# Performance work log

Hardware: AMD Instinct MI355X
Metric: run time of the kernel (lower is better)

Reference implementation:

```python
import jax, jax.numpy as jnp
import numpy as np

B, T, D, H, N, S, FF = 8, 1024, 512, 8, 256, 256, 2048
AUD, TXT = 768, 256  # audio_input_dim, text_feature_dim (hardcoded in module)
EPS = 1e-5


def _ln(x, g, b):
    m = x.mean(-1, keepdims=True)
    v = ((x - m) ** 2).mean(-1, keepdims=True)
    return (x - m) / jnp.sqrt(v + EPS) * g + b


def _lin(x, w, b):
    return x @ w + b


def setup_inputs() -> dict:
    keys = iter(jax.random.split(jax.random.key(0), 64))
    def rn(shape, s=0.02):
        return jax.random.normal(next(keys), shape, jnp.float32) * s
    inp = {
        'x': jax.random.normal(next(keys), (B, T, D), jnp.float32),
        'xf': jax.random.normal(next(keys), (B, AUD), jnp.float32),
        'xw': jax.random.normal(next(keys), (B, N, TXT), jnp.float32),
        'xs': jax.random.normal(next(keys), (B, S, D), jnp.float32),
        # feat_proj (linear variant)
        'fp_w': rn((D, D)), 'fp_b': rn((D,)),
        # self-attention
        'sa_ng': 1.0 + rn((D,)), 'sa_nb': rn((D,)),
        'sa_qw': rn((D, D)), 'sa_qb': rn((D,)),
        'sa_kw': rn((D, D)), 'sa_kb': rn((D,)),
        'sa_vw': rn((D, D)), 'sa_vb': rn((D,)),
        'sa_ow': rn((D, D)), 'sa_ob': rn((D,)),
        # cross-attention
        'ca_ng': 1.0 + rn((D,)), 'ca_nb': rn((D,)),
        'ca_tng': 1.0 + rn((D,)), 'ca_tnb': rn((D,)),
        'ca_sng': 1.0 + rn((D,)), 'ca_snb': rn((D,)),
        'ca_qw': rn((D, D)), 'ca_qb': rn((D,)),
        'ca_kw': rn((D, D)), 'ca_kb': rn((D,)),
        'ca_vw': rn((D, D)), 'ca_vb': rn((D,)),
        'ca_apw': rn((AUD, TXT)), 'ca_apb': rn((TXT,)),
        'ca_atw': rn((TXT, D)), 'ca_atb': rn((D,)),
        'ca_ow': rn((D, D)), 'ca_ob': rn((D,)),
        'an_g': 1.0 + rn((D,)), 'an_b': rn((D,)),
        # FFN
        'ffn_w1': rn((D, FF)), 'ffn_b1': rn((FF,)),
        'ffn_w2': rn((FF, D)), 'ffn_b2': rn((D,)),
        'ffn_ng': 1.0 + rn((D,)), 'ffn_nb': rn((D,)),
        'ffn_ow': rn((D, D)), 'ffn_ob': rn((D,)),
    }
    return inp


def reference(x, xf, xw, xs, fp_w, fp_b, sa_ng, sa_nb, sa_qw, sa_qb, sa_kw, sa_kb,
              sa_vw, sa_vb, sa_ow, sa_ob, ca_ng, ca_nb, ca_tng, ca_tnb, ca_sng, ca_snb,
              ca_qw, ca_qb, ca_kw, ca_kb, ca_vw, ca_vb, ca_apw, ca_apb, ca_atw, ca_atb,
              ca_ow, ca_ob, an_g, an_b, ffn_w1, ffn_b1, ffn_w2, ffn_b2, ffn_ng, ffn_nb,
              ffn_ow, ffn_ob):
    Bx, Tx, Dx = x.shape
    dh = Dx // H
    # feat_proj + detached residual (x_ori = x.detach().clone())
    xp = _lin(x, fp_w, fp_b) + jax.lax.stop_gradient(x)

    # ---- self-attention block ----
    xn = _ln(xp, sa_ng, sa_nb)
    q = _lin(xn, sa_qw, sa_qb).reshape(Bx, Tx, H, dh)
    k = _lin(xn, sa_kw, sa_kb).reshape(Bx, Tx, H, dh)
    v = _lin(xn, sa_vw, sa_vb).reshape(Bx, Tx, H, dh)
    scores = jnp.einsum('bthd,bshd->bths', q, k) / jnp.sqrt(jnp.float32(dh))
    ao = jnp.einsum('bths,bshd->bthd', jax.nn.softmax(scores, -1), v).reshape(Bx, Tx, Dx)
    sa_out = xp + _lin(jax.nn.silu(ao), sa_ow, sa_ob)
    y1 = _ln(sa_out + xp, an_g, an_b)

    # ---- cross-attention block (linear attention over text/audio + semantic) ----
    Nw = xw.shape[1]
    xf_p = _lin(xf, ca_apw, ca_apb)                              # [B, 256]
    xf_e = jnp.broadcast_to(xf_p[:, None, :], (Bx, Nw, TXT))
    xw_xf = _lin(jnp.concatenate([xw, xf_e], axis=1), ca_atw, ca_atb)  # [B, 2N, D]
    tn = _ln(xw_xf, ca_tng, ca_tnb)
    sn = _ln(xs, ca_sng, ca_snb)
    cq = jax.nn.softmax(_lin(_ln(y1, ca_ng, ca_nb), ca_qw, ca_qb).reshape(Bx, Tx, H, dh), -1)
    ck = jax.nn.softmax(_lin(tn, ca_kw, ca_kb).reshape(Bx, 2 * Nw, H, dh), 1)
    sk = jax.nn.softmax(_lin(sn, ca_kw, ca_kb).reshape(Bx, -1, H, dh), 1)
    cv = _lin(tn, ca_vw, ca_vb).reshape(Bx, 2 * Nw, H, dh)
    sv = _lin(sn, ca_vw, ca_vb).reshape(Bx, -1, H, dh)
    att = jnp.einsum('bnhd,bnhl->bhdl', ck, cv)                  # [B,H,dh,dh]
    satt = jnp.einsum('bshd,bshl->bhsl', sk, sv)                 # [B,H,S,dh]
    cy = jnp.einsum('bthd,bhdl->bthl', cq, att).reshape(Bx, Tx, Dx)
    sy = jnp.einsum('bthd,bhsl->bthl', cq, satt).reshape(Bx, Tx, Dx)
    ca_out = y1 + _lin(jax.nn.silu(cy + sy), ca_ow, ca_ob)
    y2 = _ln(ca_out + y1, an_g, an_b)

    # ---- FFN block ----
    h = jax.nn.gelu(_lin(y2, ffn_w1, ffn_b1), approximate=False)
    h = _ln(_lin(h, ffn_w2, ffn_b2), ffn_ng, ffn_nb)
    ffn_out = y2 + _lin(jax.nn.silu(h), ffn_ow, ffn_ob)
    y3 = _ln(ffn_out + y2, an_g, an_b)
    return y3
```

## Files before the change

### kernel.cpp

```cpp
#include <hip/hip_runtime.h>
#include <math.h>

typedef unsigned short u16;
typedef short s16x8 __attribute__((ext_vector_type(8)));
typedef float f32x4 __attribute__((ext_vector_type(4)));
typedef unsigned short u16x8 __attribute__((ext_vector_type(8)));
typedef unsigned short u16x4 __attribute__((ext_vector_type(4)));

#define DD 512

__device__ __forceinline__ float silu_f(float x) { return x / (1.f + __expf(-x)); }
__device__ __forceinline__ float gelu_f(float x) {
  float y = 1.5957691216f * (x + 0.044715f * x * x * x);
  return x / (1.f + __expf(-y));
}
__device__ __forceinline__ u16 f2bf(float f) {
  unsigned u = __float_as_uint(f);
  return (u16)((u + 0x7fffu + ((u >> 16) & 1u)) >> 16);
}
__device__ __forceinline__ float bf2f(u16 u) { return __uint_as_float(((unsigned)u) << 16); }
__device__ __forceinline__ unsigned cvtpk_bf16(float a, float b) {
  unsigned r;
  asm("v_cvt_pk_bf16_f32 %0, %1, %2" : "=v"(r) : "v"(a), "v"(b));
  return r;
}

__device__ __forceinline__ void gload16(const void* g, void* l) {
  __builtin_amdgcn_global_load_lds(
      (const __attribute__((address_space(1))) void*)(g),
      (__attribute__((address_space(3))) void*)(l), 16, 0, 0);
}

template<int ACT, int OB>
__global__ __launch_bounds__(256) void gemm64(
    const u16* __restrict__ A, const u16* __restrict__ Bt,
    const float* __restrict__ bias, const float* __restrict__ res, float res_scale,
    float* __restrict__ outf, float* __restrict__ outf2,
    u16* __restrict__ outb, u16* __restrict__ outb2,
    int M, int N, int K)
{
  __shared__ u16 As[2][4096];
  __shared__ u16 Bs[2][4096];
  const int t = threadIdx.x, l = t & 63, w = t >> 6;
  const int gx = gridDim.x;
  const int nblk = gx * gridDim.y;
  const int id = blockIdx.y * gx + blockIdx.x;
  const int nid = (id & 7) * (nblk >> 3) + (id >> 3);
  const int bm = (nid / gx) << 6, bn = (nid % gx) << 6;
  const int wr = (w >> 1) << 5, wc = (w & 1) << 5;
  f32x4 acc[2][2];
#pragma unroll
  for (int i = 0; i < 2; ++i)
#pragma unroll
    for (int j = 0; j < 2; ++j) acc[i][j] = (f32x4){0.f, 0.f, 0.f, 0.f};

  auto stage = [&](int k0, int buf) {
#pragma unroll
    for (int i = 0; i < 2; ++i) {
      int c = t + (i << 8);
      int row = c >> 3, cq = c & 7;
      int cs = cq ^ (row & 7);
      gload16(A + (size_t)(bm + row) * K + k0 + cs * 8, (char*)As[buf] + (i << 12) + (w << 10));
      gload16(Bt + (size_t)(bn + row) * K + k0 + cs * 8, (char*)Bs[buf] + (i << 12) + (w << 10));
    }
  };
  stage(0, 0);
  asm volatile("s_waitcnt vmcnt(0)" ::: "memory");
  __builtin_amdgcn_s_barrier();

  const int fr = l & 15, q0 = l >> 4;
  const int nk = K >> 6;
  int cur = 0;
  for (int kt = 0; kt < nk; ++kt) {
    if (kt + 1 < nk) stage((kt + 1) << 6, cur ^ 1);
    s16x8 af[2][2], bg[2][2];
#pragma unroll
    for (int kk = 0; kk < 2; ++kk)
#pragma unroll
      for (int i = 0; i < 2; ++i) {
        int ra = wr + i * 16 + fr;
        af[kk][i] = *(const s16x8*)&As[cur][ra * 64 + (((q0 + kk * 4)) ^ (ra & 7)) * 8];
        int rb = wc + i * 16 + fr;
        bg[kk][i] = *(const s16x8*)&Bs[cur][rb * 64 + (((q0 + kk * 4)) ^ (rb & 7)) * 8];
      }
    asm volatile("s_waitcnt lgkmcnt(0)" ::: "memory");
    __builtin_amdgcn_sched_barrier(0);
#pragma unroll
    for (int kk = 0; kk < 2; ++kk)
#pragma unroll
      for (int mi = 0; mi < 2; ++mi)
#pragma unroll
        for (int ni = 0; ni < 2; ++ni)
          acc[mi][ni] = __builtin_amdgcn_mfma_f32_16x16x32_bf16(af[kk][mi], bg[kk][ni], acc[mi][ni], 0, 0, 0);
    asm volatile("s_waitcnt vmcnt(0)" ::: "memory");
    __builtin_amdgcn_s_barrier();
    cur ^= 1;
  }

  const int cr0 = (l >> 4) << 2, cc = l & 15;

  if (OB == 0 || OB == 4) {
    float* fdst = outf;
    int coff = bn, ld = N;
    if (OB == 4) { ld = 512; coff = bn & 511; if (bn >= 512) fdst = outf2; }
#pragma unroll
    for (int ni = 0; ni < 2; ++ni) {
      int n = bn + wc + ni * 16 + cc;
      int col = coff + wc + ni * 16 + cc;
      float bia = bias[n];
#pragma unroll
      for (int mi = 0; mi < 2; ++mi) {
#pragma unroll
        for (int r = 0; r < 4; ++r) {
          int m = bm + wr + mi * 16 + cr0 + r;
          size_t off = (size_t)m * ld + col;
          float o = acc[mi][ni][r] + bia;
          if (ACT == 1) o = gelu_f(o);
          if (res) o = fmaf(res_scale, res[off], o);
          fdst[off] = o;
        }
      }
    }
  } else {
    int seg = bn >> 9;
    int colbase = bn & 511;
    if (seg < 2) {
      u16* dst = seg ? outb2 : outb;
#pragma unroll
      for (int ni = 0; ni < 2; ++ni) {
        int col = colbase + wc + ni * 16 + cc;
        float bia = bias[bn + wc + ni * 16 + cc];
#pragma unroll
        for (int mi = 0; mi < 2; ++mi) {
#pragma unroll
          for (int r = 0; r < 4; ++r) {
            int m = bm + wr + mi * 16 + cr0 + r;
            dst[(size_t)m * 512 + col] = f2bf(acc[mi][ni][r] + bia);
          }
        }
      }
    } else {
      u16* tile = &As[0][0];
      __syncthreads();
#pragma unroll
      for (int ni = 0; ni < 2; ++ni) {
        int lc = wc + ni * 16 + cc;
        float bia = bias[bn + wc + ni * 16 + cc];
#pragma unroll
        for (int mi = 0; mi < 2; ++mi) {
          int lm0 = wr + mi * 16 + cr0;
          u16x4 pk;
#pragma unroll
          for (int r = 0; r < 4; ++r) pk[r] = f2bf(acc[mi][ni][r] + bia);
          *(u16x4*)&tile[lc * 64 + (lm0 ^ ((lc & 7) << 3))] = pk;
        }
      }
      __syncthreads();
      int h = colbase >> 6;
      size_t vrow0 = ((size_t)((bm >> 10) * 8 + h)) * 64;
      int d = t >> 3, c8 = (t & 7) << 3;
      *(u16x8*)(((u16*)outf) + (vrow0 + d) * 1024 + (bm & 1023) + c8) =
          *(u16x8*)&tile[d * 64 + (c8 ^ ((d & 7) << 3))];
    }
  }
}

template<int ACT, int OBF>
__global__ __launch_bounds__(512) void gemm8w(
    const u16* __restrict__ A, const u16* __restrict__ Bt,
    const float* __restrict__ bias, float* __restrict__ outf, u16* __restrict__ outb,
    int M, int N, int K)
{
  __shared__ u16 As[2][4096];
  __shared__ u16 Bs[2][8192];
  const int t = threadIdx.x, l = t & 63, w = t >> 6;
  const int gx = gridDim.x;
  const int nblk = gx * gridDim.y;
  const int id = blockIdx.y * gx + blockIdx.x;
  const int nid = (id & 7) * (nblk >> 3) + (id >> 3);
  const int bm = (nid / gx) << 7, bn = (nid % gx) << 8;
  const int wr = (w >> 2) << 6, wc = (w & 3) << 6;
  f32x4 acc[4][4];
#pragma unroll
  for (int i = 0; i < 4; ++i)
#pragma unroll
    for (int j = 0; j < 4; ++j) acc[i][j] = (f32x4){0.f, 0.f, 0.f, 0.f};

  auto stage = [&](int k0, int buf) {
    {
      int row = t >> 2, kq = (t & 3) << 3;
      gload16(A + (size_t)(bm + row) * K + k0 + kq, (char*)As[buf] + (w << 10));
    }
#pragma unroll
    for (int i = 0; i < 2; ++i) {
      int c = t + (i << 9);
      int row = c >> 2, kq = (c & 3) << 3;
      gload16(Bt + (size_t)(bn + row) * K + k0 + kq, (char*)Bs[buf] + ((w + (i << 3)) << 10));
    }
  };
  stage(0, 0);
  asm volatile("s_waitcnt vmcnt(0)" ::: "memory");
  __builtin_amdgcn_s_barrier();

  const int fr = l & 15, fk = (l >> 4) << 3;
  const int nk = K >> 5;
  int cur = 0;
  for (int kt = 0; kt < nk; ++kt) {
    if (kt + 1 < nk) stage((kt + 1) << 5, cur ^ 1);
    s16x8 af[4], bg[4];
#pragma unroll
    for (int i = 0; i < 4; ++i) {
      af[i] = *(const s16x8*)&As[cur][(wr + i * 16 + fr) * 32 + fk];
      bg[i] = *(const s16x8*)&Bs[cur][(wc + i * 16 + fr) * 32 + fk];
    }
    asm volatile("s_waitcnt lgkmcnt(0)" ::: "memory");
    __builtin_amdgcn_sched_barrier(0);
#pragma unroll
    for (int mi = 0; mi < 4; ++mi)
#pragma unroll
      for (int ni = 0; ni < 4; ++ni)
        acc[mi][ni] = __builtin_amdgcn_mfma_f32_16x16x32_bf16(af[mi], bg[ni], acc[mi][ni], 0, 0, 0);
    asm volatile("s_waitcnt vmcnt(0)" ::: "memory");
    __builtin_amdgcn_s_barrier();
    cur ^= 1;
  }

  const int cr0 = (l >> 4) << 2, cc = l & 15;
#pragma unroll
  for (int ni = 0; ni < 4; ++ni) {
    int n = bn + wc + ni * 16 + cc;
    float bia = bias[n];
#pragma unroll
    for (int mi = 0; mi < 4; ++mi) {
#pragma unroll
      for (int r = 0; r < 4; ++r) {
        int m = bm + wr + mi * 16 + cr0 + r;
        size_t off = (size_t)m * N + n;
        float o = acc[mi][ni][r] + bia;
        if (ACT == 1) o = gelu_f(o);
        if (OBF) outb[off] = f2bf(o);
        else outf[off] = o;
      }
    }
  }
}

__global__ __launch_bounds__(256) void xfp_k(
    const float* __restrict__ xf, const u16* __restrict__ apwT,
    const float* __restrict__ bias, float* __restrict__ xfp)
{
  int wid = blockIdx.x * 4 + (threadIdx.x >> 6);
  int lane = threadIdx.x & 63;
  int b = wid >> 8, n = wid & 255;
  const u16* wp = apwT + (size_t)n * 768;
  const float* xp = xf + (size_t)b * 768;
  float s = 0.f;
#pragma unroll
  for (int j = 0; j < 12; ++j) s = fmaf(xp[lane + j * 64], bf2f(wp[lane + j * 64]), s);
#pragma unroll
  for (int m = 1; m < 64; m <<= 1) s += __shfl_xor(s, m);
  if (lane == 0) xfp[wid] = s + bias[n];
}

__global__ __launch_bounds__(256) void biascat_k(
    const float* __restrict__ qb, const float* __restrict__ kb, const float* __restrict__ vb,
    const float* __restrict__ ckb, const float* __restrict__ cvb,
    float* __restrict__ bQKV, float* __restrict__ bKV)
{
  int t = blockIdx.x * 256 + threadIdx.x;
  if (t < 512) bQKV[t] = qb[t];
  else if (t < 1024) bQKV[t] = kb[t - 512];
  else if (t < 1536) bQKV[t] = vb[t - 1024];
  else if (t < 2048) bKV[t - 1536] = ckb[t - 1536];
  else if (t < 2560) bKV[t - 1536] = cvb[t - 2048];
}

__global__ __launch_bounds__(256) void ln_k(
    const float* __restrict__ src, const float* __restrict__ g,
    const float* __restrict__ b, float* __restrict__ out32, u16* __restrict__ out16,
    int rows, int do_silu)
{
  int lane = threadIdx.x & 63, wv = threadIdx.x >> 6;
  int row = (blockIdx.x << 2) + wv;
  if (row >= rows) return;
  const float* p = src + (size_t)row * DD;
  float4 v0 = *(const float4*)(p + lane * 4);
  float4 v1 = *(const float4*)(p + 256 + lane * 4);
  float s = v0.x + v0.y + v0.z + v0.w + v1.x + v1.y + v1.z + v1.w;
  float ss = v0.x*v0.x + v0.y*v0.y + v0.z*v0.z + v0.w*v0.w
           + v1.x*v1.x + v1.y*v1.y + v1.z*v1.z + v1.w*v1.w;
#pragma unroll
  for (int m = 1; m < 64; m <<= 1) { s += __shfl_xor(s, m); ss += __shfl_xor(ss, m); }
  float mean = s * (1.f / 512.f);
  float var = ss * (1.f / 512.f) - mean * mean;
  float rstd = rsqrtf(var + 1e-5f);
  float4 g0 = *(const float4*)(g + lane * 4);
  float4 g1 = *(const float4*)(g + 256 + lane * 4);
  float4 b0 = *(const float4*)(b + lane * 4);
  float4 b1 = *(const float4*)(b + 256 + lane * 4);
  float o[8];
  o[0] = (v0.x - mean) * rstd * g0.x + b0.x;
  o[1] = (v0.y - mean) * rstd * g0.y + b0.y;
  o[2] = (v0.z - mean) * rstd * g0.z + b0.z;
  o[3] = (v0.w - mean) * rstd * g0.w + b0.w;
  o[4] = (v1.x - mean) * rstd * g1.x + b1.x;
  o[5] = (v1.y - mean) * rstd * g1.y + b1.y;
  o[6] = (v1.z - mean) * rstd * g1.z + b1.z;
  o[7] = (v1.w - mean) * rstd * g1.w + b1.w;
  if (do_silu) {
#pragma unroll
    for (int j = 0; j < 8; ++j) o[j] = silu_f(o[j]);
  }
  if (out32) {
    *(float4*)(out32 + (size_t)row * DD + lane * 4) = make_float4(o[0], o[1], o[2], o[3]);
    *(float4*)(out32 + (size_t)row * DD + 256 + lane * 4) = make_float4(o[4], o[5], o[6], o[7]);
  }
  if (out16) {
    u16x4 h0, h1;
#pragma unroll
    for (int j = 0; j < 4; ++j) { h0[j] = f2bf(o[j]); h1[j] = f2bf(o[4 + j]); }
    *(u16x4*)(out16 + (size_t)row * DD + lane * 4) = h0;
    *(u16x4*)(out16 + (size_t)row * DD + 256 + lane * 4) = h1;
  }
}

__global__ __launch_bounds__(256) void attn3_k(
    const u16* __restrict__ q, const u16* __restrict__ k,
    const u16* __restrict__ vt, u16* __restrict__ out)
{
  __shared__ __align__(16) char KVb[2][2][8192];
  __shared__ __align__(16) char QP[16384];
  __shared__ float Lr[4][32];

  const int t = threadIdx.x, l = t & 63, w = t >> 6;
  const int id = blockIdx.x;
  const int blk = (id & 7) * 64 + (id >> 3);
  const int qt = blk & 7, h = (blk >> 3) & 7, b = blk >> 6;
  const size_t qbase = ((size_t)(b * 1024 + qt * 128)) * 512 + h * 64;
  const size_t kbase = ((size_t)(b * 1024)) * 512 + h * 64;
  const size_t vbase = ((size_t)((b * 8 + h) * 64)) * 1024;

#pragma unroll
  for (int i = 0; i < 4; ++i) {
    int chunk = i * 256 + w * 64 + l;
    int row = chunk >> 3, c = chunk & 7;
    int cs = c ^ (row & 7);
    gload16(q + qbase + (size_t)row * 512 + cs * 8, QP + (i * 256 + w * 64) * 16);
  }
  auto stageKV = [&](int st, int buf) {
#pragma unroll
    for (int i = 0; i < 2; ++i) {
      int chunk = i * 256 + w * 64 + l;
      int row = chunk >> 3, c = chunk & 7;
      int cs = c ^ (row & 7);
      gload16(k + kbase + (size_t)(st * 64 + row) * 512 + cs * 8,
              KVb[buf][0] + (i * 256 + w * 64) * 16);
      gload16(vt + vbase + (size_t)row * 1024 + st * 64 + cs * 8,
              KVb[buf][1] + (i * 256 + w * 64) * 16);
    }
  };
  stageKV(0, 0);
  __syncthreads();

  s16x8 qf[2][2];
#pragma unroll
  for (int ti = 0; ti < 2; ++ti)
#pragma unroll
    for (int kk = 0; kk < 2; ++kk) {
      int row = w * 32 + ti * 16 + (l & 15);
      int ch = ((l >> 4) + kk * 4) ^ (row & 7);
      qf[ti][kk] = *(const s16x8*)(QP + row * 128 + ch * 16);
    }

  f32x4 oacc[2][4];
#pragma unroll
  for (int qi = 0; qi < 2; ++qi)
#pragma unroll
    for (int dj = 0; dj < 4; ++dj) oacc[qi][dj] = (f32x4){0.f, 0.f, 0.f, 0.f};
  float lsum[2] = {0.f, 0.f};

  int cur = 0;
  for (int st = 0; st < 16; ++st) {
    if (st + 1 < 16) stageKV(st + 1, cur ^ 1);
    f32x4 sacc[4][2];
#pragma unroll
    for (int si = 0; si < 4; ++si)
#pragma unroll
      for (int ti = 0; ti < 2; ++ti) sacc[si][ti] = (f32x4){0.f, 0.f, 0.f, 0.f};
#pragma unroll
    for (int si = 0; si < 4; ++si) {
#pragma unroll
      for (int kk = 0; kk < 2; ++kk) {
        int s = si * 16 + (l & 15);
        int ch = ((l >> 4) + kk * 4) ^ (s & 7);
        s16x8 kf = *(const s16x8*)(KVb[cur][0] + s * 128 + ch * 16);
#pragma unroll
        for (int ti = 0; ti < 2; ++ti)
          sacc[si][ti] = __builtin_amdgcn_mfma_f32_16x16x32_bf16(kf, qf[ti][kk], sacc[si][ti], 0, 0, 0);
      }
    }
#pragma unroll
    for (int si = 0; si < 4; ++si)
#pragma unroll
      for (int ti = 0; ti < 2; ++ti) {
        float e0 = __expf(sacc[si][ti][0] * 0.125f);
        float e1 = __expf(sacc[si][ti][1] * 0.125f);
        float e2 = __expf(sacc[si][ti][2] * 0.125f);
        float e3 = __expf(sacc[si][ti][3] * 0.125f);
        lsum[ti] += (e0 + e1) + (e2 + e3);
        uint2 pk2;
        pk2.x = cvtpk_bf16(e0, e1);
        pk2.y = cvtpk_bf16(e2, e3);
        int tl = ti * 16 + (l & 15);
        int sb = (si * 16 + (l >> 4) * 4) * 2;
        *(uint2*)(QP + w * 4096 + tl * 128 + (sb ^ ((tl & 7) << 4))) = pk2;
      }
#pragma unroll
    for (int kk = 0; kk < 2; ++kk) {
      s16x8 pf[2];
#pragma unroll
      for (int qi = 0; qi < 2; ++qi) {
        int tl = qi * 16 + (l & 15);
        int ch = ((l >> 4) + kk * 4) ^ (tl & 7);
        pf[qi] = *(const s16x8*)(QP + w * 4096 + tl * 128 + ch * 16);
      }
#pragma unroll
      for (int dj = 0; dj < 4; ++dj) {
        int d = dj * 16 + (l & 15);
        int ch = ((l >> 4) + kk * 4) ^ (d & 7);
        s16x8 vf = *(const s16x8*)(KVb[cur][1] + d * 128 + ch * 16);
#pragma unroll
        for (int qi = 0; qi < 2; ++qi)
          oacc[qi][dj] = __builtin_amdgcn_mfma_f32_16x16x32_bf16(pf[qi], vf, oacc[qi][dj], 0, 0, 0);
      }
    }
    cur ^= 1;
    __syncthreads();
  }

#pragma unroll
  for (int ti = 0; ti < 2; ++ti) {
    lsum[ti] += __shfl_xor(lsum[ti], 16);
    lsum[ti] += __shfl_xor(lsum[ti], 32);
    Lr[w][ti * 16 + (l & 15)] = lsum[ti];
  }
  __syncthreads();
  u16* otile = (u16*)QP;
#pragma unroll
  for (int qi = 0; qi < 2; ++qi) {
    float linv[4];
#pragma unroll
    for (int r = 0; r < 4; ++r) linv[r] = 1.f / Lr[w][qi * 16 + (l >> 4) * 4 + r];
#pragma unroll
    for (int dj = 0; dj < 4; ++dj) {
#pragma unroll
      for (int r = 0; r < 4; ++r) {
        int trl = w * 32 + qi * 16 + (l >> 4) * 4 + r;
        otile[trl * 64 + dj * 16 + (l & 15)] = f2bf(silu_f(oacc[qi][dj][r] * linv[r]));
      }
    }
  }
  __syncthreads();
#pragma unroll
  for (int p = 0; p < 4; ++p) {
    int flat = p * 256 + t;
    int row = flat >> 3, c8 = (flat & 7) << 3;
    *(u16x8*)(out + ((size_t)(b * 1024 + qt * 128 + row)) * 512 + h * 64 + c8) =
        *(u16x8*)&otile[row * 64 + c8];
  }
}

__global__ __launch_bounds__(256) void softmax64_k(float* __restrict__ p, int rows)
{
  int lane = threadIdx.x & 63, wv = threadIdx.x >> 6;
  int row = (blockIdx.x << 2) + wv;
  if (row >= rows) return;
  float x = p[(size_t)row * 64 + lane];
  float m = x;
#pragma unroll
  for (int mk = 1; mk < 64; mk <<= 1) m = fmaxf(m, __shfl_xor(m, mk));
  float e = __expf(x - m);
  float s = e;
#pragma unroll
  for (int mk = 1; mk < 64; mk <<= 1) s += __shfl_xor(s, mk);
  p[(size_t)row * 64 + lane] = e / s;
}

template<int NL>
__global__ __launch_bounds__(256) void smseq_k(float* __restrict__ p)
{
  __shared__ float red[256];
  int t = threadIdx.x;
  int ci = t & 15, nj = t >> 4;
  int b = blockIdx.x >> 5, cg = blockIdx.x & 31;
  int col = cg * 16 + ci;
  float vals[NL / 16];
  float s = 0.f;
#pragma unroll
  for (int j = 0; j < NL / 16; ++j) {
    float x = __expf(p[((size_t)(b * NL) + nj + j * 16) * 512 + col]);
    vals[j] = x; s += x;
  }
  red[t] = s;
  __syncthreads();
  float tot = 0.f;
#pragma unroll
  for (int j = 0; j < 16; ++j) tot += red[ci + j * 16];
  float inv = 1.f / tot;
#pragma unroll
  for (int j = 0; j < NL / 16; ++j)
    p[((size_t)(b * NL) + nj + j * 16) * 512 + col] = vals[j] * inv;
}

__global__ __launch_bounds__(256) void build_xc_k(
    const float* __restrict__ xw, const float* __restrict__ xfp, u16* __restrict__ xc)
{
  int idx = blockIdx.x * 256 + threadIdx.x;
  int c = idx & 255, n = (idx >> 8) & 511, b = idx >> 17;
  float val = (n < 256) ? xw[((b << 8) + n) * 256 + c] : xfp[(b << 8) + c];
  xc[idx] = f2bf(val);
}

__global__ __launch_bounds__(256) void attmat1_k(
    const float* __restrict__ ckp, const float* __restrict__ cvp, float* __restrict__ attp)
{
  __shared__ float a_s[64][68];
  __shared__ float b_s[64][68];
  int bh = blockIdx.x >> 3, sl = blockIdx.x & 7;
  int h = bh & 7, b = bh >> 3;
  int n0 = sl << 6;
  int tid = threadIdx.x;
  int d = tid & 63, lg = tid >> 6;
  float acc[16];
#pragma unroll
  for (int j = 0; j < 16; ++j) acc[j] = 0.f;
#pragma unroll
  for (int i = 0; i < 4; ++i) {
    int f = tid + (i << 8);
    int row = f >> 4, c4 = (f & 15) << 2;
    size_t src = ((size_t)(b * 512 + n0 + row)) * DD + h * 64 + c4;
    *(float4*)&a_s[row][c4] = *(const float4*)(ckp + src);
    *(float4*)&b_s[row][c4] = *(const float4*)(cvp + src);
  }
  __syncthreads();
  for (int nn = 0; nn < 64; ++nn) {
    float av = a_s[nn][d];
#pragma unroll
    for (int j4 = 0; j4 < 4; ++j4) {
      float4 b4 = *(float4*)&b_s[nn][lg * 16 + j4 * 4];
      acc[j4*4+0] = fmaf(av, b4.x, acc[j4*4+0]);
      acc[j4*4+1] = fmaf(av, b4.y, acc[j4*4+1]);
      acc[j4*4+2] = fmaf(av, b4.z, acc[j4*4+2]);
      acc[j4*4+3] = fmaf(av, b4.w, acc[j4*4+3]);
    }
  }
  float* op = attp + ((size_t)(bh * 8 + sl)) * 4096 + d * 64 + lg * 16;
#pragma unroll
  for (int j4 = 0; j4 < 4; ++j4)
    *(float4*)(op + j4 * 4) = make_float4(acc[j4*4+0], acc[j4*4+1], acc[j4*4+2], acc[j4*4+3]);
}

__global__ __launch_bounds__(256) void attred_k(
    const float* __restrict__ attp, float* __restrict__ att)
{
  int idx = (blockIdx.x * 256 + threadIdx.x) * 4;
  int bh = idx >> 12, e = idx & 4095;
  float4 s = make_float4(0.f, 0.f, 0.f, 0.f);
#pragma unroll
  for (int sl = 0; sl < 8; ++sl) {
    float4 v = *(const float4*)&attp[((size_t)(bh * 8 + sl)) * 4096 + e];
    s.x += v.x; s.y += v.y; s.z += v.z; s.w += v.w;
  }
  *(float4*)&att[idx] = s;
}

__global__ __launch_bounds__(256) void rowsum64_k(
    const float* __restrict__ skp, float* __restrict__ r)
{
  int wv = threadIdx.x >> 6, l = threadIdx.x & 63;
  int g16 = l >> 4, l16 = l & 15;
  for (int it = 0; it < 16; ++it) {
    int rid = blockIdx.x * 256 + wv * 64 + it * 4 + g16;
    const float* base = skp + (size_t)(rid >> 3) * 512 + (rid & 7) * 64;
    float4 v = *(const float4*)(base + l16 * 4);
    float s = (v.x + v.y) + (v.z + v.w);
    s += __shfl_xor(s, 1); s += __shfl_xor(s, 2);
    s += __shfl_xor(s, 4); s += __shfl_xor(s, 8);
    if (l16 == 0) r[rid] = s;
  }
}

__global__ __launch_bounds__(256) void sy2_k(
    const float* __restrict__ r, const float* __restrict__ svp, float* __restrict__ sy)
{
  __shared__ float part[4][64];
  int b = blockIdx.x >> 3, h = blockIdx.x & 7;
  int t = threadIdx.x;
  int li = t & 63, sg = t >> 6;
  float acc = 0.f;
  for (int j = 0; j < 64; ++j) {
    int s = sg * 64 + j;
    size_t ix = (size_t)(b * 256 + s);
    acc = fmaf(r[ix * 8 + h], svp[ix * 512 + h * 64 + li], acc);
  }
  part[sg][li] = acc;
  __syncthreads();
  if (t < 64) sy[(b * 8 + h) * 64 + t] = (part[0][t] + part[1][t]) + (part[2][t] + part[3][t]);
}

__global__ __launch_bounds__(256) void cy_k(
    const float* __restrict__ cq, const float* __restrict__ att,
    const float* __restrict__ sy, u16* __restrict__ out)
{
  __shared__ float atts[64][68];
  __shared__ float qs[64][68];
  __shared__ float sys[64];
  int blk = blockIdx.x;
  int tt = blk & 15, h = (blk >> 4) & 7, b = blk >> 7;
  int t0 = tt << 6;
  int tid = threadIdx.x;
#pragma unroll
  for (int i = 0; i < 4; ++i) {
    int f = tid + (i << 8);
    int row = f >> 4, c4 = (f & 15) << 2;
    *(float4*)&atts[row][c4] = *(const float4*)(att + (size_t)(b * 8 + h) * 4096 + row * 64 + c4);
    *(float4*)&qs[row][c4] = *(const float4*)(cq + ((size_t)(b * 1024 + t0 + row)) * DD + h * 64 + c4);
  }
  if (tid < 64) sys[tid] = sy[(b * 8 + h) * 64 + tid];
  __syncthreads();
  int r = tid >> 2, lg = tid & 3;
  float acc[16];
#pragma unroll
  for (int j = 0; j < 16; ++j) acc[j] = 0.f;
  for (int d = 0; d < 64; ++d) {
    float qv = qs[r][d];
#pragma unroll
    for (int j4 = 0; j4 < 4; ++j4) {
      float4 a4 = *(float4*)&atts[d][lg * 16 + j4 * 4];
      acc[j4*4+0] = fmaf(qv, a4.x, acc[j4*4+0]);
      acc[j4*4+1] = fmaf(qv, a4.y, acc[j4*4+1]);
      acc[j4*4+2] = fmaf(qv, a4.z, acc[j4*4+2]);
      acc[j4*4+3] = fmaf(qv, a4.w, acc[j4*4+3]);
    }
  }
  u16* op = out + ((size_t)(b * 1024 + t0 + r)) * DD + h * 64 + lg * 16;
#pragma unroll
  for (int j4 = 0; j4 < 4; ++j4) {
    u16x4 o4;
    o4[0] = f2bf(silu_f(acc[j4*4+0] + sys[lg * 16 + j4*4+0]));
    o4[1] = f2bf(silu_f(acc[j4*4+1] + sys[lg * 16 + j4*4+1]));
    o4[2] = f2bf(silu_f(acc[j4*4+2] + sys[lg * 16 + j4*4+2]));
    o4[3] = f2bf(silu_f(acc[j4*4+3] + sys[lg * 16 + j4*4+3]));
    *(u16x4*)(op + j4 * 4) = o4;
  }
}

__global__ __launch_bounds__(256) void cvtf2b_k(const float* __restrict__ in, u16* __restrict__ out, int n)
{
  int i = (blockIdx.x * 256 + threadIdx.x) * 4;
  if (i >= n) return;
  float4 v = *(const float4*)(in + i);
  u16x4 o;
  o[0] = f2bf(v.x); o[1] = f2bf(v.y); o[2] = f2bf(v.z); o[3] = f2bf(v.w);
  *(u16x4*)(out + i) = o;
}

__global__ __launch_bounds__(256) void wtrans_k(const float* __restrict__ W, u16* __restrict__ Wt, int Kd, int Nd)
{
  __shared__ float tile[32][33];
  int ntn = Nd >> 5;
  int tk = blockIdx.x / ntn, tn = blockIdx.x % ntn;
  int lx = threadIdx.x & 31, ly = threadIdx.x >> 5;
#pragma unroll
  for (int i = 0; i < 4; ++i)
    tile[ly + 8 * i][lx] = W[(size_t)(tk * 32 + ly + 8 * i) * Nd + tn * 32 + lx];
  __syncthreads();
#pragma unroll
  for (int i = 0; i < 4; ++i)
    Wt[(size_t)(tn * 32 + ly + 8 * i) * Kd + tk * 32 + lx] = f2bf(tile[lx][ly + 8 * i]);
}

struct W10 { const float* w[10]; u16* o[10]; };
__global__ __launch_bounds__(256) void wtrans10_k(W10 p)
{
  __shared__ float tile[32][33];
  int wi = blockIdx.x >> 8;
  int tb = blockIdx.x & 255;
  int tk = tb >> 4, tn = tb & 15;
  const float* W = p.w[wi];
  u16* Wt = p.o[wi];
  int lx = threadIdx.x & 31, ly = threadIdx.x >> 5;
#pragma unroll
  for (int i = 0; i < 4; ++i)
    tile[ly + 8 * i][lx] = W[(size_t)(tk * 32 + ly + 8 * i) * 512 + tn * 32 + lx];
  __syncthreads();
#pragma unroll
  for (int i = 0; i < 4; ++i)
    Wt[(size_t)(tn * 32 + ly + 8 * i) * 512 + tk * 32 + lx] = f2bf(tile[lx][ly + 8 * i]);
}

extern "C" void kernel_launch(void* const* d_in, const int* in_sizes, int n_in,
                              void* d_out, int out_size, void* d_ws, size_t ws_size,
                              hipStream_t stream)
{
  const float* x      = (const float*)d_in[0];
  const float* xf     = (const float*)d_in[1];
  const float* xw     = (const float*)d_in[2];
  const float* xs     = (const float*)d_in[3];
  const float* fp_w   = (const float*)d_in[4];
  const float* fp_b   = (const float*)d_in[5];
  const float* sa_ng  = (const float*)d_in[6];
  const float* sa_nb  = (const float*)d_in[7];
  const float* sa_qw  = (const float*)d_in[8];
  const float* sa_qb  = (const float*)d_in[9];
  const float* sa_kw  = (const float*)d_in[10];
  const float* sa_kb  = (const float*)d_in[11];
  const float* sa_vw  = (const float*)d_in[12];
  const float* sa_vb  = (const float*)d_in[13];
  const float* sa_ow  = (const float*)d_in[14];
  const float* sa_ob  = (const float*)d_in[15];
  const float* ca_ng  = (const float*)d_in[16];
  const float* ca_nb  = (const float*)d_in[17];
  const float* ca_tng = (const float*)d_in[18];
  const float* ca_tnb = (const float*)d_in[19];
  const float* ca_sng = (const float*)d_in[20];
  const float* ca_snb = (const float*)d_in[21];
  const float* ca_qw  = (const float*)d_in[22];
  const float* ca_qb  = (const float*)d_in[23];
  const float* ca_kw  = (const float*)d_in[24];
  const float* ca_kb  = (const float*)d_in[25];
  const float* ca_vw  = (const float*)d_in[26];
  const float* ca_vb  = (const float*)d_in[27];
  const float* ca_apw = (const float*)d_in[28];
  const float* ca_apb = (const float*)d_in[29];
  const float* ca_atw = (const float*)d_in[30];
  const float* ca_atb = (const float*)d_in[31];
  const float* ca_ow  = (const float*)d_in[32];
  const float* ca_ob  = (const float*)d_in[33];
  const float* an_g   = (const float*)d_in[34];
  const float* an_b   = (const float*)d_in[35];
  const float* ffn_w1 = (const float*)d_in[36];
  const float* ffn_b1 = (const float*)d_in[37];
  const float* ffn_w2 = (const float*)d_in[38];
  const float* ffn_b2 = (const float*)d_in[39];
  const float* ffn_ng = (const float*)d_in[40];
  const float* ffn_nb = (const float*)d_in[41];
  const float* ffn_ow = (const float*)d_in[42];
  const float* ffn_ob = (const float*)d_in[43];

  float* ws = (float*)d_ws;
  float* slotZ = ws;
  float* slotP = ws + 4194304;
  u16* S1 = (u16*)(ws + 8388608);
  u16* S2 = (u16*)(ws + 10485760);
  u16* S3 = (u16*)(ws + 12582912);
  u16* S4 = (u16*)(ws + 14680064);
  u16* Vt = (u16*)(ws + 16777216);
  u16* S6 = (u16*)(ws + 18874368);
  float* ck  = ws + 20971520;
  float* sk  = ws + 23068672;
  float* cv  = ws + 24117248;
  float* sv  = ws + 26214400;
  float* tnr = ws + 27262976;
  u16* tn = (u16*)(ws + 29360128);
  u16* sn = (u16*)(ws + 30408704);
  u16* h1 = (u16*)(ws + 20971520);
  u16* xc = (u16*)(ws + 30932992);
  float* att = ws + 31457280;
  float* xfp = ws + 31719424;
  float* sy  = ws + 31723520;
  u16* wb = (u16*)(ws + 31727616);
  u16* fp_wt   = wb;
  u16* sa_qwt  = wb + 262144;
  u16* sa_kwt  = wb + 524288;
  u16* sa_vwt  = wb + 786432;
  u16* sa_owt  = wb + 1048576;
  u16* ca_qwt  = wb + 1310720;
  u16* ca_kwt  = wb + 1572864;
  u16* ca_vwt  = wb + 1835008;
  u16* ca_owt  = wb + 2097152;
  u16* ffn_owt = wb + 2359296;
  u16* ca_atwt = wb + 2621440;
  u16* ffn_w1t = wb + 2752512;
  u16* ffn_w2t = wb + 3801088;
  u16* apwT    = wb + 4849664;
  float* bQKV  = (float*)(wb + 5046272);
  float* bKV   = bQKV + 1536;
  float* attp  = ws + 34260992;
  float* rws   = ws + 36358144;

  dim3 blk(256);
  auto g64 = [](int M, int N) { return dim3((unsigned)(N >> 6), (unsigned)(M >> 6)); };

  cvtf2b_k<<<dim3(4096), blk, 0, stream>>>(x, S1, 4194304);
  W10 wp;
  wp.w[0] = fp_w;  wp.o[0] = fp_wt;
  wp.w[1] = sa_qw; wp.o[1] = sa_qwt;
  wp.w[2] = sa_kw; wp.o[2] = sa_kwt;
  wp.w[3] = sa_vw; wp.o[3] = sa_vwt;
  wp.w[4] = sa_ow; wp.o[4] = sa_owt;
  wp.w[5] = ca_qw; wp.o[5] = ca_qwt;
  wp.w[6] = ca_kw; wp.o[6] = ca_kwt;
  wp.w[7] = ca_vw; wp.o[7] = ca_vwt;
  wp.w[8] = ca_ow; wp.o[8] = ca_owt;
  wp.w[9] = ffn_ow; wp.o[9] = ffn_owt;
  wtrans10_k<<<dim3(2560), blk, 0, stream>>>(wp);
  wtrans_k<<<dim3(128), blk, 0, stream>>>(ca_atw, ca_atwt, 256, 512);
  wtrans_k<<<dim3(1024), blk, 0, stream>>>(ffn_w1, ffn_w1t, 512, 2048);
  wtrans_k<<<dim3(1024), blk, 0, stream>>>(ffn_w2, ffn_w2t, 2048, 512);
  wtrans_k<<<dim3(192), blk, 0, stream>>>(ca_apw, apwT, 768, 256);
  biascat_k<<<dim3(10), blk, 0, stream>>>(sa_qb, sa_kb, sa_vb, ca_kb, ca_vb, bQKV, bKV);

  xfp_k<<<dim3(512), blk, 0, stream>>>(xf, apwT, ca_apb, xfp);
  build_xc_k<<<dim3(4096), blk, 0, stream>>>(xw, xfp, xc);
  gemm64<0,0><<<g64(4096, 512), blk, 0, stream>>>(xc, ca_atwt, ca_atb, nullptr, 0.f, tnr, nullptr, nullptr, nullptr, 4096, 512, 256);
  ln_k<<<dim3(1024), blk, 0, stream>>>(tnr, ca_tng, ca_tnb, nullptr, tn, 4096, 0);
  ln_k<<<dim3(512), blk, 0, stream>>>(xs, ca_sng, ca_snb, nullptr, sn, 2048, 0);

  gemm64<0,0><<<g64(8192, 512), blk, 0, stream>>>(S1, fp_wt, fp_b, x, 1.f, slotP, nullptr, nullptr, nullptr, 8192, 512, 512);
  ln_k<<<dim3(2048), blk, 0, stream>>>(slotP, sa_ng, sa_nb, nullptr, S2, 8192, 0);
  gemm64<0,3><<<g64(8192, 1536), blk, 0, stream>>>(S2, sa_qwt, bQKV, nullptr, 0.f, (float*)Vt, nullptr, S3, S4, 8192, 1536, 512);
  attn3_k<<<dim3(512), blk, 0, stream>>>(S3, S4, Vt, S6);
  gemm64<0,0><<<g64(8192, 512), blk, 0, stream>>>(S6, sa_owt, sa_ob, slotP, 2.f, slotZ, nullptr, nullptr, nullptr, 8192, 512, 512);
  ln_k<<<dim3(2048), blk, 0, stream>>>(slotZ, an_g, an_b, slotP, nullptr, 8192, 0);

  ln_k<<<dim3(2048), blk, 0, stream>>>(slotP, ca_ng, ca_nb, nullptr, S1, 8192, 0);
  gemm64<0,0><<<g64(8192, 512), blk, 0, stream>>>(S1, ca_qwt, ca_qb, nullptr, 0.f, slotZ, nullptr, nullptr, nullptr, 8192, 512, 512);
  softmax64_k<<<dim3(16384), blk, 0, stream>>>(slotZ, 65536);
  gemm64<0,4><<<g64(6144, 1024), blk, 0, stream>>>(tn, ca_kwt, bKV, nullptr, 0.f, ck, cv, nullptr, nullptr, 6144, 1024, 512);
  smseq_k<512><<<dim3(256), blk, 0, stream>>>(ck);
  smseq_k<256><<<dim3(256), blk, 0, stream>>>(sk);
  attmat1_k<<<dim3(512), blk, 0, stream>>>(ck, cv, attp);
  attred_k<<<dim3(256), blk, 0, stream>>>(attp, att);
  rowsum64_k<<<dim3(64), blk, 0, stream>>>(sk, rws);
  sy2_k<<<dim3(64), blk, 0, stream>>>(rws, sv, sy);
  cy_k<<<dim3(1024), blk, 0, stream>>>(slotZ, att, sy, S2);
  gemm64<0,0><<<g64(8192, 512), blk, 0, stream>>>(S2, ca_owt, ca_ob, slotP, 2.f, slotZ, nullptr, nullptr, nullptr, 8192, 512, 512);
  ln_k<<<dim3(2048), blk, 0, stream>>>(slotZ, an_g, an_b, slotP, S3, 8192, 0);

  gemm8w<1,1><<<dim3(8, 64), dim3(512), 0, stream>>>(S3, ffn_w1t, ffn_b1, nullptr, h1, 8192, 2048, 512);
  gemm64<0,0><<<g64(8192, 512), blk, 0, stream>>>(h1, ffn_w2t, ffn_b2, nullptr, 0.f, slotZ, nullptr, nullptr, nullptr, 8192, 512, 2048);
  ln_k<<<dim3(2048), blk, 0, stream>>>(slotZ, ffn_ng, ffn_nb, nullptr, S1, 8192, 1);
  gemm64<0,0><<<g64(8192, 512), blk, 0, stream>>>(S1, ffn_owt, ffn_ob, slotP, 2.f, slotZ, nullptr, nullptr, nullptr, 8192, 512, 512);
  ln_k<<<dim3(2048), blk, 0, stream>>>(slotZ, an_g, an_b, (float*)d_out, nullptr, 8192, 0);
}
```

Before: 354.1 us.

## Store GEMM outputs as bf16, fuse back-to-back LayerNorms, swizzle gemm8w LDS

GEMM epilogues that feed a LayerNorm now write bf16 instead of fp32 through new OB=1/5 paths. The following LayerNorms read bf16 through new lnb_k/ln2_k kernels, which cuts intermediate HBM traffic. Two consecutive LayerNorms (AddNorm then cross-attention norm) are fused into one kernel, removing a launch and a full round trip. The 8-wave GEMM's LDS tiles get an XOR swizzle to cut bank conflicts. The risk is extra rounding error from storing pre-norm activations in bf16.

```diff
diff --git a/kernel.cpp b/kernel.cpp
--- a/kernel.cpp
+++ b/kernel.cpp
@@ -121,6 +121,24 @@
         }
       }
     }
+  } else if (OB == 1 || OB == 5) {
+#pragma unroll
+    for (int ni = 0; ni < 2; ++ni) {
+      int n = bn + wc + ni * 16 + cc;
+      float bia = bias[n];
+#pragma unroll
+      for (int mi = 0; mi < 2; ++mi) {
+#pragma unroll
+        for (int r = 0; r < 4; ++r) {
+          int m = bm + wr + mi * 16 + cr0 + r;
+          size_t off = (size_t)m * N + n;
+          float o = acc[mi][ni][r] + bia;
+          if (ACT == 1) o = gelu_f(o);
+          if (OB == 5) o = fmaf(res_scale, res[off], o);
+          outb[off] = f2bf(o);
+        }
+      }
+    }
   } else {
     int seg = bn >> 9;
     int colbase = bn & 511;
@@ -188,21 +206,23 @@
 
   auto stage = [&](int k0, int buf) {
     {
-      int row = t >> 2, kq = (t & 3) << 3;
-      gload16(A + (size_t)(bm + row) * K + k0 + kq, (char*)As[buf] + (w << 10));
+      int row = t >> 2, cq = t & 3;
+      int cs = cq ^ ((row >> 1) & 3);
+      gload16(A + (size_t)(bm + row) * K + k0 + cs * 8, (char*)As[buf] + (w << 10));
     }
 #pragma unroll
     for (int i = 0; i < 2; ++i) {
       int c = t + (i << 9);
-      int row = c >> 2, kq = (c & 3) << 3;
-      gload16(Bt + (size_t)(bn + row) * K + k0 + kq, (char*)Bs[buf] + ((w + (i << 3)) << 10));
+      int row = c >> 2, cq = c & 3;
+      int cs = cq ^ ((row >> 1) & 3);
+      gload16(Bt + (size_t)(bn + row) * K + k0 + cs * 8, (char*)Bs[buf] + ((w + (i << 3)) << 10));
     }
   };
   stage(0, 0);
   asm volatile("s_waitcnt vmcnt(0)" ::: "memory");
   __builtin_amdgcn_s_barrier();
 
-  const int fr = l & 15, fk = (l >> 4) << 3;
+  const int fr = l & 15, q0 = l >> 4;
   const int nk = K >> 5;
   int cur = 0;
   for (int kt = 0; kt < nk; ++kt) {
@@ -210,8 +230,10 @@
     s16x8 af[4], bg[4];
 #pragma unroll
     for (int i = 0; i < 4; ++i) {
-      af[i] = *(const s16x8*)&As[cur][(wr + i * 16 + fr) * 32 + fk];
-      bg[i] = *(const s16x8*)&Bs[cur][(wc + i * 16 + fr) * 32 + fk];
+      int ra = wr + i * 16 + fr;
+      af[i] = *(const s16x8*)&As[cur][ra * 32 + (q0 ^ ((ra >> 1) & 3)) * 8];
+      int rb = wc + i * 16 + fr;
+      bg[i] = *(const s16x8*)&Bs[cur][rb * 32 + (q0 ^ ((rb >> 1) & 3)) * 8];
     }
     asm volatile("s_waitcnt lgkmcnt(0)" ::: "memory");
     __builtin_amdgcn_sched_barrier(0);
@@ -322,6 +344,118 @@
     *(u16x4*)(out16 + (size_t)row * DD + lane * 4) = h0;
     *(u16x4*)(out16 + (size_t)row * DD + 256 + lane * 4) = h1;
   }
+}
+
+__global__ __launch_bounds__(256) void lnb_k(
+    const u16* __restrict__ src, const float* __restrict__ g,
+    const float* __restrict__ b, float* __restrict__ out32, u16* __restrict__ out16,
+    int rows, int do_silu)
+{
+  int lane = threadIdx.x & 63, wv = threadIdx.x >> 6;
+  int row = (blockIdx.x << 2) + wv;
+  if (row >= rows) return;
+  const u16* p = src + (size_t)row * DD;
+  u16x4 a0 = *(const u16x4*)(p + lane * 4);
+  u16x4 a1 = *(const u16x4*)(p + 256 + lane * 4);
+  float v[8];
+#pragma unroll
+  for (int j = 0; j < 4; ++j) { v[j] = bf2f(a0[j]); v[4 + j] = bf2f(a1[j]); }
+  float s = 0.f, ss = 0.f;
+#pragma unroll
+  for (int j = 0; j < 8; ++j) { s += v[j]; ss = fmaf(v[j], v[j], ss); }
+#pragma unroll
+  for (int m = 1; m < 64; m <<= 1) { s += __shfl_xor(s, m); ss += __shfl_xor(ss, m); }
+  float mean = s * (1.f / 512.f);
+  float var = ss * (1.f / 512.f) - mean * mean;
+  float rstd = rsqrtf(var + 1e-5f);
+  float4 g0 = *(const float4*)(g + lane * 4);
+  float4 g1 = *(const float4*)(g + 256 + lane * 4);
+  float4 b0 = *(const float4*)(b + lane * 4);
+  float4 b1 = *(const float4*)(b + 256 + lane * 4);
+  float o[8];
+  o[0] = (v[0] - mean) * rstd * g0.x + b0.x;
+  o[1] = (v[1] - mean) * rstd * g0.y + b0.y;
+  o[2] = (v[2] - mean) * rstd * g0.z + b0.z;
+  o[3] = (v[3] - mean) * rstd * g0.w + b0.w;
+  o[4] = (v[4] - mean) * rstd * g1.x + b1.x;
+  o[5] = (v[5] - mean) * rstd * g1.y + b1.y;
+  o[6] = (v[6] - mean) * rstd * g1.z + b1.z;
+  o[7] = (v[7] - mean) * rstd * g1.w + b1.w;
+  if (do_silu) {
+#pragma unroll
+    for (int j = 0; j < 8; ++j) o[j] = silu_f(o[j]);
+  }
+  if (out32) {
+    *(float4*)(out32 + (size_t)row * DD + lane * 4) = make_float4(o[0], o[1], o[2], o[3]);
+    *(float4*)(out32 + (size_t)row * DD + 256 + lane * 4) = make_float4(o[4], o[5], o[6], o[7]);
+  }
+  if (out16) {
+    u16x4 h0, h1;
+#pragma unroll
+    for (int j = 0; j < 4; ++j) { h0[j] = f2bf(o[j]); h1[j] = f2bf(o[4 + j]); }
+    *(u16x4*)(out16 + (size_t)row * DD + lane * 4) = h0;
+    *(u16x4*)(out16 + (size_t)row * DD + 256 + lane * 4) = h1;
+  }
+}
+
+__global__ __launch_bounds__(256) void ln2_k(
+    const u16* __restrict__ src, const float* __restrict__ g1, const float* __restrict__ b1,
+    const float* __restrict__ g2, const float* __restrict__ b2,
+    float* __restrict__ out1, u16* __restrict__ out2, int rows)
+{
+  int lane = threadIdx.x & 63, wv = threadIdx.x >> 6;
+  int row = (blockIdx.x << 2) + wv;
+  if (row >= rows) return;
+  const u16* p = src + (size_t)row * DD;
+  u16x4 a0 = *(const u16x4*)(p + lane * 4);
+  u16x4 a1 = *(const u16x4*)(p + 256 + lane * 4);
+  float v[8];
+#pragma unroll
+  for (int j = 0; j < 4; ++j) { v[j] = bf2f(a0[j]); v[4 + j] = bf2f(a1[j]); }
+  float s = 0.f, ss = 0.f;
+#pragma unroll
+  for (int j = 0; j < 8; ++j) { s += v[j]; ss = fmaf(v[j], v[j], ss); }
+#pragma unroll
+  for (int m = 1; m < 64; m <<= 1) { s += __shfl_xor(s, m); ss += __shfl_xor(ss, m); }
+  float mean = s * (1.f / 512.f);
+  float rstd = rsqrtf(ss * (1.f / 512.f) - mean * mean + 1e-5f);
+  float4 G0 = *(const float4*)(g1 + lane * 4);
+  float4 G1 = *(const float4*)(g1 + 256 + lane * 4);
+  float4 B0 = *(const float4*)(b1 + lane * 4);
+  float4 B1 = *(const float4*)(b1 + 256 + lane * 4);
+  float y[8];
+  y[0] = (v[0] - mean) * rstd * G0.x + B0.x;
+  y[1] = (v[1] - mean) * rstd * G0.y + B0.y;
+  y[2] = (v[2] - mean) * rstd * G0.z + B0.z;
+  y[3] = (v[3] - mean) * rstd * G0.w + B0.w;
+  y[4] = (v[4] - mean) * rstd * G1.x + B1.x;
+  y[5] = (v[5] - mean) * rstd * G1.y + B1.y;
+  y[6] = (v[6] - mean) * rstd * G1.z + B1.z;
+  y[7] = (v[7] - mean) * rstd * G1.w + B1.w;
+  *(float4*)(out1 + (size_t)row * DD + lane * 4) = make_float4(y[0], y[1], y[2], y[3]);
+  *(float4*)(out1 + (size_t)row * DD + 256 + lane * 4) = make_float4(y[4], y[5], y[6], y[7]);
+  float s2 = 0.f, ss2 = 0.f;
+#pragma unroll
+  for (int j = 0; j < 8; ++j) { s2 += y[j]; ss2 = fmaf(y[j], y[j], ss2); }
+#pragma unroll
+  for (int m = 1; m < 64; m <<= 1) { s2 += __shfl_xor(s2, m); ss2 += __shfl_xor(ss2, m); }
+  float m2 = s2 * (1.f / 512.f);
+  float r2 = rsqrtf(ss2 * (1.f / 512.f) - m2 * m2 + 1e-5f);
+  float4 H0 = *(const float4*)(g2 + lane * 4);
+  float4 H1 = *(const float4*)(g2 + 256 + lane * 4);
+  float4 C0 = *(const float4*)(b2 + lane * 4);
+  float4 C1 = *(const float4*)(b2 + 256 + lane * 4);
+  u16x4 h0, h1;
+  h0[0] = f2bf((y[0] - m2) * r2 * H0.x + C0.x);
+  h0[1] = f2bf((y[1] - m2) * r2 * H0.y + C0.y);
+  h0[2] = f2bf((y[2] - m2) * r2 * H0.z + C0.z);
+  h0[3] = f2bf((y[3] - m2) * r2 * H0.w + C0.w);
+  h1[0] = f2bf((y[4] - m2) * r2 * H1.x + C1.x);
+  h1[1] = f2bf((y[5] - m2) * r2 * H1.y + C1.y);
+  h1[2] = f2bf((y[6] - m2) * r2 * H1.z + C1.z);
+  h1[3] = f2bf((y[7] - m2) * r2 * H1.w + C1.w);
+  *(u16x4*)(out2 + (size_t)row * DD + lane * 4) = h0;
+  *(u16x4*)(out2 + (size_t)row * DD + 256 + lane * 4) = h1;
 }
 
 __global__ __launch_bounds__(256) void attn3_k(
@@ -751,6 +885,7 @@
   float* ws = (float*)d_ws;
   float* slotZ = ws;
   float* slotP = ws + 4194304;
+  u16* Zb = (u16*)slotZ;
   u16* S1 = (u16*)(ws + 8388608);
   u16* S2 = (u16*)(ws + 10485760);
   u16* S3 = (u16*)(ws + 12582912);
@@ -821,10 +956,9 @@
   ln_k<<<dim3(2048), blk, 0, stream>>>(slotP, sa_ng, sa_nb, nullptr, S2, 8192, 0);
   gemm64<0,3><<<g64(8192, 1536), blk, 0, stream>>>(S2, sa_qwt, bQKV, nullptr, 0.f, (float*)Vt, nullptr, S3, S4, 8192, 1536, 512);
   attn3_k<<<dim3(512), blk, 0, stream>>>(S3, S4, Vt, S6);
-  gemm64<0,0><<<g64(8192, 512), blk, 0, stream>>>(S6, sa_owt, sa_ob, slotP, 2.f, slotZ, nullptr, nullptr, nullptr, 8192, 512, 512);
-  ln_k<<<dim3(2048), blk, 0, stream>>>(slotZ, an_g, an_b, slotP, nullptr, 8192, 0);
-
-  ln_k<<<dim3(2048), blk, 0, stream>>>(slotP, ca_ng, ca_nb, nullptr, S1, 8192, 0);
+  gemm64<0,5><<<g64(8192, 512), blk, 0, stream>>>(S6, sa_owt, sa_ob, slotP, 2.f, nullptr, nullptr, Zb, nullptr, 8192, 512, 512);
+  ln2_k<<<dim3(2048), blk, 0, stream>>>(Zb, an_g, an_b, ca_ng, ca_nb, slotP, S1, 8192);
+
   gemm64<0,0><<<g64(8192, 512), blk, 0, stream>>>(S1, ca_qwt, ca_qb, nullptr, 0.f, slotZ, nullptr, nullptr, nullptr, 8192, 512, 512);
   softmax64_k<<<dim3(16384), blk, 0, stream>>>(slotZ, 65536);
   gemm64<0,4><<<g64(6144, 1024), blk, 0, stream>>>(tn, ca_kwt, bKV, nullptr, 0.f, ck, cv, nullptr, nullptr, 6144, 1024, 512);
@@ -835,12 +969,12 @@
   rowsum64_k<<<dim3(64), blk, 0, stream>>>(sk, rws);
   sy2_k<<<dim3(64), blk, 0, stream>>>(rws, sv, sy);
   cy_k<<<dim3(1024), blk, 0, stream>>>(slotZ, att, sy, S2);
-  gemm64<0,0><<<g64(8192, 512), blk, 0, stream>>>(S2, ca_owt, ca_ob, slotP, 2.f, slotZ, nullptr, nullptr, nullptr, 8192, 512, 512);
-  ln_k<<<dim3(2048), blk, 0, stream>>>(slotZ, an_g, an_b, slotP, S3, 8192, 0);
+  gemm64<0,5><<<g64(8192, 512), blk, 0, stream>>>(S2, ca_owt, ca_ob, slotP, 2.f, nullptr, nullptr, Zb, nullptr, 8192, 512, 512);
+  lnb_k<<<dim3(2048), blk, 0, stream>>>(Zb, an_g, an_b, slotP, S3, 8192, 0);
 
   gemm8w<1,1><<<dim3(8, 64), dim3(512), 0, stream>>>(S3, ffn_w1t, ffn_b1, nullptr, h1, 8192, 2048, 512);
-  gemm64<0,0><<<g64(8192, 512), blk, 0, stream>>>(h1, ffn_w2t, ffn_b2, nullptr, 0.f, slotZ, nullptr, nullptr, nullptr, 8192, 512, 2048);
-  ln_k<<<dim3(2048), blk, 0, stream>>>(slotZ, ffn_ng, ffn_nb, nullptr, S1, 8192, 1);
-  gemm64<0,0><<<g64(8192, 512), blk, 0, stream>>>(S1, ffn_owt, ffn_ob, slotP, 2.f, slotZ, nullptr, nullptr, nullptr, 8192, 512, 512);
-  ln_k<<<dim3(2048), blk, 0, stream>>>(slotZ, an_g, an_b, (float*)d_out, nullptr, 8192, 0);
-}
+  gemm64<0,1><<<g64(8192, 512), blk, 0, stream>>>(h1, ffn_w2t, ffn_b2, nullptr, 0.f, nullptr, nullptr, Zb, nullptr, 8192, 512, 2048);
+  lnb_k<<<dim3(2048), blk, 0, stream>>>(Zb, ffn_ng, ffn_nb, nullptr, S1, 8192, 1);
+  gemm64<0,5><<<g64(8192, 512), blk, 0, stream>>>(S1, ffn_owt, ffn_ob, slotP, 2.f, nullptr, nullptr, Zb, nullptr, 8192, 512, 512);
+  lnb_k<<<dim3(2048), blk, 0, stream>>>(Zb, an_g, an_b, (float*)d_out, nullptr, 8192, 0);
+}
```

Result: faster. 339.4 us (-4.2%).
